# Performance work log

Hardware: AMD Instinct MI355X
Metric: run time of the kernel (lower is better)

The kernel has to match this reference:

```python
import jax, jax.numpy as jnp
import numpy as np

NUM_OUT_EDGES = 2
NUM_INTERMEDIATE = 2
NUM_FSM_STATES = NUM_OUT_EDGES + NUM_INTERMEDIATE  # S = 4
NUM_EDGE_TYPES = 3
NUM_VARIANTS = 4
NUM_NODE_TYPES = 8
NUM_NODES = 256
BACKTRACK_FAILS_PROB = 0.001
EDGE_PROB = 0.05  # avg degree ~ 12.8 per edge type


def setup_inputs() -> dict:
    key = jax.random.key(0)
    k1, k2, k3, k4 = jax.random.split(key, 4)
    vw = jax.random.uniform(k1, (NUM_NODES, NUM_NODES, NUM_VARIANTS))
    vw = vw / jnp.sum(vw, axis=-1, keepdims=True)  # nonneg, sums to 1 on last axis
    adjacency = (jax.random.uniform(k2, (NUM_EDGE_TYPES, NUM_NODES, NUM_NODES)) < EDGE_PROB).astype(jnp.float32)
    n_actions = NUM_EDGE_TYPES * NUM_FSM_STATES + 3  # moves + ACCEPT/BACKTRACK/FAIL
    log_routing_params = 0.5 * jax.random.normal(
        k3, (NUM_VARIANTS, NUM_NODE_TYPES, NUM_FSM_STATES, n_actions))
    node_types = jax.random.randint(k4, (NUM_NODES,), 0, NUM_NODE_TYPES)
    return {
        'variant_weights': vw,
        'adjacency': adjacency,
        'log_routing_params': log_routing_params,
        'node_types': node_types,
        'steps': 48,
    }


def _forward(variant_weights, adjacency, log_routing_params, node_types, steps):
    N = variant_weights.shape[0]
    S, T, E = NUM_FSM_STATES, NUM_EDGE_TYPES, NUM_OUT_EDGES
    dt = variant_weights.dtype

    # Row-normalized per-edge-type adjacency (uniform over typed successors;
    deg = jnp.sum(adjacency, axis=-1, keepdims=True)
    a_norm = adjacency / jnp.maximum(deg, 1.0)  # [T, N, N]

    # routing_softmax over actions; policy conditioned on (variant, node type, fsm state)
    policy = jax.nn.softmax(log_routing_params, axis=-1)  # [V, NT, S, A]
    pol_n = policy[:, node_types]                          # [V, N, S, A]

    # Mix policy variants per (start node i, current node j)
    mixed = jnp.einsum('ijv,vjsa->ijsa', variant_weights, pol_n)  # [N, N, S, A]
    p_move = mixed[..., :T * S].reshape(N, N, S, T, S)  # MOVE(edge type t, next state u)
    p_accept = mixed[..., T * S]                        # ACCEPT at current node
    p_back = mixed[..., T * S + 1]                      # BACKTRACK to start node

    # Start states: edge type e starts in fsm state e at node i (one-hot).
    eyeS = jnp.eye(S, dtype=dt)[:E]  # [E, S]
    eyeN = jnp.eye(N, dtype=dt)      # [N, N]
    dist0 = eyeS[:, None, :, None] * eyeN[None, :, None, :]  # [E, N, S, N]
    restart = dist0 * (1.0 - BACKTRACK_FAILS_PROB)

    def step(carry, _):
        dist, accept = carry  # dist: [E, N_start, S, N_cur], accept: [E, N, N]
        accept = accept + jnp.einsum('eisj,ijs->eij', dist, p_accept)
        back = jnp.einsum('eisj,ijs->ei', dist, p_back)
        tmp = jnp.einsum('eisj,ijstu->eituj', dist, p_move)   # pick edge type + next state
        moved = jnp.einsum('eituj,tjk->eiuk', tmp, a_norm)    # move along typed edges
        dist = moved + back[:, :, None, None] * restart
        return (dist, accept), None

    accept0 = jnp.zeros((E, N, N), dt)
    (dist, accept), _ = jax.lax.scan(step, (dist0, accept0), None, length=steps)
    # absorb remaining accept probability after final transition
    accept = accept + jnp.einsum('eisj,ijs->eij', dist, p_accept)
    return accept  # [num_out_edges, num_nodes, num_nodes]


def reference(variant_weights, adjacency, log_routing_params, node_types, steps):
    return _forward(variant_weights, adjacency, log_routing_params, node_types, steps)
```

## Files before the change

### kernel.cpp

```cpp
#include <hip/hip_runtime.h>
#include <hip/hip_fp16.h>

#define NN    256
#define SS    4
#define TT    3
#define VV    4
#define NTY   8
#define NAC   15
#define CAPG  48
#define CAPE  (CAPG * 2)
#define ROWB  40
#define ZROWB (NN * ROWB)
#define BUFB  (ZROWB + ROWB)
#define ZPK   ((unsigned)ZROWB | ((unsigned)ZROWB << 16))
#define GMR   16

typedef _Float16 h2v __attribute__((ext_vector_type(2)));

#if defined(__has_builtin)
#if __has_builtin(__builtin_amdgcn_fdot2)
#define HAVE_FDOT2 1
#endif
#endif

static __device__ __forceinline__ unsigned ph2(float a, float b) {
    union { __half2 h; unsigned u; } c;
    c.h = __floats2half2_rn(a, b);
    return c.u;
}
static __device__ __forceinline__ h2v bch2(unsigned u) {
    union { unsigned u; h2v h; } c; c.u = u; return c.h;
}
static __device__ __forceinline__ float2 h2f2(unsigned u) {
    union { unsigned u; __half2 h; } c; c.u = u; return __half22float2(c.h);
}

__global__ void k_setup(const float* __restrict__ adj,
                        const float* __restrict__ lrp,
                        float* __restrict__ inv_deg,
                        float* __restrict__ pol,
                        unsigned* __restrict__ epk,
                        int* __restrict__ gcnt) {
    const int b = blockIdx.x;
    const int tid = threadIdx.x;

    if (b < TT * NN) {
        __shared__ float wsum[4];
        float s = adj[(size_t)b * NN + tid];
#pragma unroll
        for (int off = 32; off > 0; off >>= 1) s += __shfl_down(s, off, 64);
        if ((tid & 63) == 0) wsum[tid >> 6] = s;
        __syncthreads();
        if (tid == 0)
            inv_deg[b] = 1.0f / fmaxf(wsum[0] + wsum[1] + wsum[2] + wsum[3], 1.0f);
    } else if (b < TT * NN + 64) {
        __shared__ int cnt[4];
        __shared__ unsigned short offs[4][CAPE + 2];
        const int c4 = (b - TT * NN) * 4;
        if (tid < 4) cnt[tid] = 0;
        __syncthreads();
#pragma unroll
        for (int t = 0; t < TT; t++) {
            const float4 a4 = *(const float4*)(adj + ((size_t)t * NN + tid) * NN + c4);
            const float av[4] = {a4.x, a4.y, a4.z, a4.w};
#pragma unroll
            for (int c = 0; c < 4; c++) {
                if (av[c] != 0.f) {
                    int idx = atomicAdd(&cnt[c], 1);
                    if (idx < CAPE) offs[c][idx] = (unsigned short)(tid * ROWB + t * 8);
                }
            }
        }
        __syncthreads();
        const int c    = tid >> 6;
        const int lane = tid & 63;
        int cc = cnt[c]; if (cc > CAPE) cc = CAPE;
        if (lane == 0 && (cc & 1)) offs[c][cc] = (unsigned short)ZROWB;
        __syncthreads();
        const int g = (cc + 1) >> 1;
        for (int gg = lane; gg < g; gg += 64)
            epk[(size_t)gg * NN + (c4 + c)] =
                (unsigned)offs[c][2 * gg] | ((unsigned)offs[c][2 * gg + 1] << 16);
        if (lane == 0) gcnt[c4 + c] = g;
    } else {
        if (tid < VV * NTY * SS) {
            float x[NAC]; float m = -3.4e38f;
#pragma unroll
            for (int a = 0; a < NAC; a++) { x[a] = lrp[tid * NAC + a]; m = fmaxf(m, x[a]); }
            float ssum = 0.f;
#pragma unroll
            for (int a = 0; a < NAC; a++) { x[a] = __expf(x[a] - m); ssum += x[a]; }
            float inv = 1.f / ssum;
#pragma unroll
            for (int a = 0; a < NAC; a++) pol[tid * NAC + a] = x[a] * inv;
        }
    }
}

__global__ __launch_bounds__(512, 4) void k_main(
    const float* __restrict__ vw,
    const int* __restrict__ node_types,
    const float* __restrict__ pol,
    const float* __restrict__ inv_deg,
    const unsigned* __restrict__ epk,
    const int* __restrict__ gcnt,
    const int* __restrict__ steps_p,
    float* __restrict__ out)
{
    const int i    = blockIdx.x & 255;
    const int e    = blockIdx.x >> 8;
    const int tid  = threadIdx.x;
    const int col  = tid >> 1;
    const int h    = tid & 1;
    const int lane = tid & 63;
    const int wv   = tid >> 6;
    const int steps = steps_p[0];

    __shared__ __align__(16) char tmpb[2 * BUFB];
    __shared__ __align__(16) float backp[2][8];

    if (tid < 20) {
        int pb = tid / 10, w = tid % 10;
        ((unsigned*)(tmpb + pb * BUFB + ZROWB))[w] = 0u;
    }

    const float4 w4 = *(const float4*)(vw + ((size_t)i * NN + col) * VV);
    const float wvv[VV] = {w4.x, w4.y, w4.z, w4.w};
    const int ntj = node_types[col];
    const int ab  = h * 6;
    float pm6[SS][6], pcb[SS];
#pragma unroll
    for (int s = 0; s < SS; s++) {
        pcb[s] = 0.f;
#pragma unroll
        for (int a = 0; a < 6; a++) pm6[s][a] = 0.f;
    }
#pragma unroll
    for (int v = 0; v < VV; v++) {
        const float* pr = pol + (size_t)(v * NTY + ntj) * SS * NAC;
#pragma unroll
        for (int s = 0; s < SS; s++) {
            const float* p = pr + s * NAC;
#pragma unroll
            for (int a = 0; a < 6; a++) pm6[s][a] = fmaf(wvv[v], p[ab + a], pm6[s][a]);
            pcb[s] = fmaf(wvv[v], p[12 + h], pcb[s]);
        }
    }
    {
        float invd[TT];
#pragma unroll
        for (int t = 0; t < TT; t++) invd[t] = inv_deg[t * NN + col];
#pragma unroll
        for (int s = 0; s < SS; s++)
#pragma unroll
            for (int a = 0; a < 6; a++) pm6[s][a] *= invd[(ab + a) >> 2];
    }

    float D0 = (0 == e && col == i) ? 1.f : 0.f;
    float D1 = (1 == e && col == i) ? 1.f : 0.f;
    float D2 = 0.f, D3 = 0.f;
    float acc = 0.f;

    const int g_all = gcnt[col];
    const int ch = (g_all - h + 1) >> 1;
    int km = ch;
#pragma unroll
    for (int off = 32; off > 0; off >>= 1) {
        int o = __shfl_xor(km, off, 64);
        km = o > km ? o : km;
    }
    const int kmax = __builtin_amdgcn_readfirstlane(km);

    unsigned ep[GMR];
#pragma unroll
    for (int k = 0; k < GMR; k++) {
        unsigned pk = epk[(size_t)(2 * k + h) * NN + col];
        ep[k] = (2 * k + h < g_all) ? pk : ZPK;
    }

    const h2v S10 = {(_Float16)1.0f, (_Float16)0.0f};
    const h2v S01 = {(_Float16)0.0f, (_Float16)1.0f};
    char* const myrow0 = tmpb + col * ROWB + h * 12;

    for (int step = 0; step < steps; step++) {
        const int par = step & 1;
        char* const buf = tmpb + par * BUFB;

        float r4 = D0 * pcb[0];
        r4 = fmaf(D1, pcb[1], r4); r4 = fmaf(D2, pcb[2], r4); r4 = fmaf(D3, pcb[3], r4);
        if (h == 0) acc += r4;
        float bj = h ? r4 : 0.f;

        float tv[6];
#pragma unroll
        for (int a = 0; a < 6; a++) {
            float x = D0 * pm6[0][a];
            x = fmaf(D1, pm6[1][a], x);
            x = fmaf(D2, pm6[2][a], x);
            x = fmaf(D3, pm6[3][a], x);
            tv[a] = x;
        }
        char* const myrow = myrow0 + par * BUFB;
        *(unsigned*)(myrow)     = ph2(tv[0], tv[1]);
        *(unsigned*)(myrow + 4) = ph2(tv[2], tv[3]);
        *(unsigned*)(myrow + 8) = ph2(tv[4], tv[5]);

#pragma unroll
        for (int off = 32; off > 0; off >>= 1) bj += __shfl_down(bj, off, 64);
        if (lane == 0) backp[par][wv] = bj;

        __syncthreads();

        float d0a = 0.f, d1a = 0.f, d2a = 0.f, d3a = 0.f;
        float d0b = 0.f, d1b = 0.f, d2b = 0.f, d3b = 0.f;
#pragma unroll
        for (int k = 0; k < GMR; k++) {
            if (k < kmax) {
                const unsigned pk = ep[k];
                const uint2 q0 = *(const uint2*)(buf + (pk & 0xffffu));
                const uint2 q1 = *(const uint2*)(buf + (pk >> 16));
#ifdef HAVE_FDOT2
                if (k & 1) {
                    d0b = __builtin_amdgcn_fdot2(bch2(q0.x), S10, d0b, false);
                    d1b = __builtin_amdgcn_fdot2(bch2(q0.x), S01, d1b, false);
                    d2b = __builtin_amdgcn_fdot2(bch2(q0.y), S10, d2b, false);
                    d3b = __builtin_amdgcn_fdot2(bch2(q0.y), S01, d3b, false);
                    d0b = __builtin_amdgcn_fdot2(bch2(q1.x), S10, d0b, false);
                    d1b = __builtin_amdgcn_fdot2(bch2(q1.x), S01, d1b, false);
                    d2b = __builtin_amdgcn_fdot2(bch2(q1.y), S10, d2b, false);
                    d3b = __builtin_amdgcn_fdot2(bch2(q1.y), S01, d3b, false);
                } else {
                    d0a = __builtin_amdgcn_fdot2(bch2(q0.x), S10, d0a, false);
                    d1a = __builtin_amdgcn_fdot2(bch2(q0.x), S01, d1a, false);
                    d2a = __builtin_amdgcn_fdot2(bch2(q0.y), S10, d2a, false);
                    d3a = __builtin_amdgcn_fdot2(bch2(q0.y), S01, d3a, false);
                    d0a = __builtin_amdgcn_fdot2(bch2(q1.x), S10, d0a, false);
                    d1a = __builtin_amdgcn_fdot2(bch2(q1.x), S01, d1a, false);
                    d2a = __builtin_amdgcn_fdot2(bch2(q1.y), S10, d2a, false);
                    d3a = __builtin_amdgcn_fdot2(bch2(q1.y), S01, d3a, false);
                }
#else
                float2 f0 = h2f2(q0.x), f1 = h2f2(q0.y), f2 = h2f2(q1.x), f3 = h2f2(q1.y);
                if (k & 1) {
                    d0b += f0.x + f2.x; d1b += f0.y + f2.y;
                    d2b += f1.x + f3.x; d3b += f1.y + f3.y;
                } else {
                    d0a += f0.x + f2.x; d1a += f0.y + f2.y;
                    d2a += f1.x + f3.x; d3a += f1.y + f3.y;
                }
#endif
            }
        }
        for (int k = GMR; k < kmax; k++) {
            unsigned pk = epk[(size_t)(2 * k + h) * NN + col];
            pk = (2 * k + h < g_all) ? pk : ZPK;
            const uint2 q0 = *(const uint2*)(buf + (pk & 0xffffu));
            const uint2 q1 = *(const uint2*)(buf + (pk >> 16));
            float2 f0 = h2f2(q0.x), f1 = h2f2(q0.y), f2 = h2f2(q1.x), f3 = h2f2(q1.y);
            d0a += f0.x + f2.x; d1a += f0.y + f2.y;
            d2a += f1.x + f3.x; d3a += f1.y + f3.y;
        }

        float d0 = d0a + d0b, d1 = d1a + d1b, d2 = d2a + d2b, d3 = d3a + d3b;

        d0 += __shfl_xor(d0, 1, 64);
        d1 += __shfl_xor(d1, 1, 64);
        d2 += __shfl_xor(d2, 1, 64);
        d3 += __shfl_xor(d3, 1, 64);

        const float4 b0 = *(const float4*)(&backp[par][0]);
        const float4 b1 = *(const float4*)(&backp[par][4]);
        const float back = ((b0.x + b0.y) + (b0.z + b0.w)) +
                           ((b1.x + b1.y) + (b1.z + b1.w));
        if (col == i) {
            if (e == 0) d0 = fmaf(back, 0.999f, d0);
            else        d1 = fmaf(back, 0.999f, d1);
        }
        D0 = d0; D1 = d1; D2 = d2; D3 = d3;
    }

    float r4 = D0 * pcb[0];
    r4 = fmaf(D1, pcb[1], r4); r4 = fmaf(D2, pcb[2], r4); r4 = fmaf(D3, pcb[3], r4);
    if (h == 0) {
        acc += r4;
        out[((size_t)e * NN + i) * NN + col] = acc;
    }
}

extern "C" void kernel_launch(void* const* d_in, const int* in_sizes, int n_in,
                              void* d_out, int out_size, void* d_ws, size_t ws_size,
                              hipStream_t stream) {
    const float* vw  = (const float*)d_in[0];
    const float* adj = (const float*)d_in[1];
    const float* lrp = (const float*)d_in[2];
    const int* node_types = (const int*)d_in[3];
    const int* steps_p    = (const int*)d_in[4];

    float* ws       = (float*)d_ws;
    float* pol      = ws;
    float* inv_deg  = ws + 1920;
    int*   gcnt     = (int*)(ws + 2688);
    unsigned* epk   = (unsigned*)(ws + 2944);

    k_setup<<<TT * NN + 64 + 1, 256, 0, stream>>>(adj, lrp, inv_deg, pol, epk, gcnt);
    k_main<<<2 * NN, 512, 0, stream>>>(vw, node_types, pol, inv_deg, epk, gcnt,
                                       steps_p, (float*)d_out);
}
```

Measured before the change: 166.6 us.

## Split each destination column across four threads instead of two

Moves from 2 to 4 threads per column (1024-thread blocks). Three lanes each handle one edge type's move probabilities and edge-group gathers, and the fourth computes the accept and backtrack terms. This shortens each thread's serial per-step gather chain and spreads the work over more waves. The cost is an extra cross-lane shuffle round, a larger block-wide barrier and fewer registers per thread.

```diff
diff --git a/kernel.cpp b/kernel.cpp
--- a/kernel.cpp
+++ b/kernel.cpp
@@ -13,7 +13,7 @@
 #define ZROWB (NN * ROWB)
 #define BUFB  (ZROWB + ROWB)
 #define ZPK   ((unsigned)ZROWB | ((unsigned)ZROWB << 16))
-#define GMR   16
+#define GMR4  8
 
 typedef _Float16 h2v __attribute__((ext_vector_type(2)));
 
@@ -97,7 +97,7 @@
     }
 }
 
-__global__ __launch_bounds__(512, 4) void k_main(
+__global__ __launch_bounds__(1024, 8) void k_main(
     const float* __restrict__ vw,
     const int* __restrict__ node_types,
     const float* __restrict__ pol,
@@ -110,14 +110,14 @@
     const int i    = blockIdx.x & 255;
     const int e    = blockIdx.x >> 8;
     const int tid  = threadIdx.x;
-    const int col  = tid >> 1;
-    const int h    = tid & 1;
+    const int col  = tid >> 2;
+    const int h    = tid & 3;
     const int lane = tid & 63;
     const int wv   = tid >> 6;
     const int steps = steps_p[0];
 
     __shared__ __align__(16) char tmpb[2 * BUFB];
-    __shared__ __align__(16) float backp[2][8];
+    __shared__ __align__(16) float backp[2][16];
 
     if (tid < 20) {
         int pb = tid / 10, w = tid % 10;
@@ -127,14 +127,14 @@
     const float4 w4 = *(const float4*)(vw + ((size_t)i * NN + col) * VV);
     const float wvv[VV] = {w4.x, w4.y, w4.z, w4.w};
     const int ntj = node_types[col];
-    const int ab  = h * 6;
-    float pm6[SS][6], pcb[SS];
-#pragma unroll
-    for (int s = 0; s < SS; s++) {
-        pcb[s] = 0.f;
-#pragma unroll
-        for (int a = 0; a < 6; a++) pm6[s][a] = 0.f;
-    }
+    int ai[4];
+    if (h < 3) { ai[0] = 4 * h; ai[1] = 4 * h + 1; ai[2] = 4 * h + 2; ai[3] = 4 * h + 3; }
+    else       { ai[0] = 12;    ai[1] = 13;        ai[2] = 14;        ai[3] = 14;        }
+    float pm[SS][4];
+#pragma unroll
+    for (int s = 0; s < SS; s++)
+#pragma unroll
+        for (int u = 0; u < 4; u++) pm[s][u] = 0.f;
 #pragma unroll
     for (int v = 0; v < VV; v++) {
         const float* pr = pol + (size_t)(v * NTY + ntj) * SS * NAC;
@@ -142,18 +142,16 @@
         for (int s = 0; s < SS; s++) {
             const float* p = pr + s * NAC;
 #pragma unroll
-            for (int a = 0; a < 6; a++) pm6[s][a] = fmaf(wvv[v], p[ab + a], pm6[s][a]);
-            pcb[s] = fmaf(wvv[v], p[12 + h], pcb[s]);
+            for (int u = 0; u < 4; u++) pm[s][u] = fmaf(wvv[v], p[ai[u]], pm[s][u]);
         }
     }
     {
-        float invd[TT];
-#pragma unroll
-        for (int t = 0; t < TT; t++) invd[t] = inv_deg[t * NN + col];
+        float invd = 1.f;
+        if (h < 3) invd = inv_deg[h * NN + col];
 #pragma unroll
         for (int s = 0; s < SS; s++)
 #pragma unroll
-            for (int a = 0; a < 6; a++) pm6[s][a] *= invd[(ab + a) >> 2];
+            for (int u = 0; u < 4; u++) pm[s][u] *= invd;
     }
 
     float D0 = (0 == e && col == i) ? 1.f : 0.f;
@@ -162,7 +160,7 @@
     float acc = 0.f;
 
     const int g_all = gcnt[col];
-    const int ch = (g_all - h + 1) >> 1;
+    const int ch = (g_all - h + 3) >> 2;
     int km = ch;
 #pragma unroll
     for (int off = 32; off > 0; off >>= 1) {
@@ -171,39 +169,36 @@
     }
     const int kmax = __builtin_amdgcn_readfirstlane(km);
 
-    unsigned ep[GMR];
-#pragma unroll
-    for (int k = 0; k < GMR; k++) {
-        unsigned pk = epk[(size_t)(2 * k + h) * NN + col];
-        ep[k] = (2 * k + h < g_all) ? pk : ZPK;
+    unsigned ep[GMR4];
+#pragma unroll
+    for (int k = 0; k < GMR4; k++) {
+        unsigned pk = epk[(size_t)(4 * k + h) * NN + col];
+        ep[k] = (4 * k + h < g_all) ? pk : ZPK;
     }
 
     const h2v S10 = {(_Float16)1.0f, (_Float16)0.0f};
     const h2v S01 = {(_Float16)0.0f, (_Float16)1.0f};
-    char* const myrow0 = tmpb + col * ROWB + h * 12;
+    char* const myrow0 = tmpb + col * ROWB + h * 8;
 
     for (int step = 0; step < steps; step++) {
         const int par = step & 1;
         char* const buf = tmpb + par * BUFB;
 
-        float r4 = D0 * pcb[0];
-        r4 = fmaf(D1, pcb[1], r4); r4 = fmaf(D2, pcb[2], r4); r4 = fmaf(D3, pcb[3], r4);
-        if (h == 0) acc += r4;
-        float bj = h ? r4 : 0.f;
-
-        float tv[6];
-#pragma unroll
-        for (int a = 0; a < 6; a++) {
-            float x = D0 * pm6[0][a];
-            x = fmaf(D1, pm6[1][a], x);
-            x = fmaf(D2, pm6[2][a], x);
-            x = fmaf(D3, pm6[3][a], x);
-            tv[a] = x;
-        }
-        char* const myrow = myrow0 + par * BUFB;
-        *(unsigned*)(myrow)     = ph2(tv[0], tv[1]);
-        *(unsigned*)(myrow + 4) = ph2(tv[2], tv[3]);
-        *(unsigned*)(myrow + 8) = ph2(tv[4], tv[5]);
+        float tv0 = D0 * pm[0][0];
+        tv0 = fmaf(D1, pm[1][0], tv0); tv0 = fmaf(D2, pm[2][0], tv0); tv0 = fmaf(D3, pm[3][0], tv0);
+        float tv1 = D0 * pm[0][1];
+        tv1 = fmaf(D1, pm[1][1], tv1); tv1 = fmaf(D2, pm[2][1], tv1); tv1 = fmaf(D3, pm[3][1], tv1);
+        float tv2 = D0 * pm[0][2];
+        tv2 = fmaf(D1, pm[1][2], tv2); tv2 = fmaf(D2, pm[2][2], tv2); tv2 = fmaf(D3, pm[3][2], tv2);
+        float tv3 = D0 * pm[0][3];
+        tv3 = fmaf(D1, pm[1][3], tv3); tv3 = fmaf(D2, pm[2][3], tv3); tv3 = fmaf(D3, pm[3][3], tv3);
+
+        float bj = 0.f;
+        if (h == 3) { acc += tv0; bj = tv1; }
+        else {
+            uint2 w; w.x = ph2(tv0, tv1); w.y = ph2(tv2, tv3);
+            *(uint2*)(myrow0 + par * BUFB) = w;
+        }
 
 #pragma unroll
         for (int off = 32; off > 0; off >>= 1) bj += __shfl_down(bj, off, 64);
@@ -214,7 +209,7 @@
         float d0a = 0.f, d1a = 0.f, d2a = 0.f, d3a = 0.f;
         float d0b = 0.f, d1b = 0.f, d2b = 0.f, d3b = 0.f;
 #pragma unroll
-        for (int k = 0; k < GMR; k++) {
+        for (int k = 0; k < GMR4; k++) {
             if (k < kmax) {
                 const unsigned pk = ep[k];
                 const uint2 q0 = *(const uint2*)(buf + (pk & 0xffffu));
@@ -251,9 +246,9 @@
 #endif
             }
         }
-        for (int k = GMR; k < kmax; k++) {
-            unsigned pk = epk[(size_t)(2 * k + h) * NN + col];
-            pk = (2 * k + h < g_all) ? pk : ZPK;
+        for (int k = GMR4; k < kmax; k++) {
+            unsigned pk = epk[(size_t)(4 * k + h) * NN + col];
+            pk = (4 * k + h < g_all) ? pk : ZPK;
             const uint2 q0 = *(const uint2*)(buf + (pk & 0xffffu));
             const uint2 q1 = *(const uint2*)(buf + (pk >> 16));
             float2 f0 = h2f2(q0.x), f1 = h2f2(q0.y), f2 = h2f2(q1.x), f3 = h2f2(q1.y);
@@ -263,15 +258,19 @@
 
         float d0 = d0a + d0b, d1 = d1a + d1b, d2 = d2a + d2b, d3 = d3a + d3b;
 
-        d0 += __shfl_xor(d0, 1, 64);
-        d1 += __shfl_xor(d1, 1, 64);
-        d2 += __shfl_xor(d2, 1, 64);
-        d3 += __shfl_xor(d3, 1, 64);
+        d0 += __shfl_xor(d0, 1, 64);  d0 += __shfl_xor(d0, 2, 64);
+        d1 += __shfl_xor(d1, 1, 64);  d1 += __shfl_xor(d1, 2, 64);
+        d2 += __shfl_xor(d2, 1, 64);  d2 += __shfl_xor(d2, 2, 64);
+        d3 += __shfl_xor(d3, 1, 64);  d3 += __shfl_xor(d3, 2, 64);
 
         const float4 b0 = *(const float4*)(&backp[par][0]);
         const float4 b1 = *(const float4*)(&backp[par][4]);
-        const float back = ((b0.x + b0.y) + (b0.z + b0.w)) +
-                           ((b1.x + b1.y) + (b1.z + b1.w));
+        const float4 b2 = *(const float4*)(&backp[par][8]);
+        const float4 b3 = *(const float4*)(&backp[par][12]);
+        const float back = (((b0.x + b0.y) + (b0.z + b0.w)) +
+                            ((b1.x + b1.y) + (b1.z + b1.w))) +
+                           (((b2.x + b2.y) + (b2.z + b2.w)) +
+                            ((b3.x + b3.y) + (b3.z + b3.w)));
         if (col == i) {
             if (e == 0) d0 = fmaf(back, 0.999f, d0);
             else        d1 = fmaf(back, 0.999f, d1);
@@ -279,10 +278,10 @@
         D0 = d0; D1 = d1; D2 = d2; D3 = d3;
     }
 
-    float r4 = D0 * pcb[0];
-    r4 = fmaf(D1, pcb[1], r4); r4 = fmaf(D2, pcb[2], r4); r4 = fmaf(D3, pcb[3], r4);
-    if (h == 0) {
-        acc += r4;
+    if (h == 3) {
+        float r = D0 * pm[0][0];
+        r = fmaf(D1, pm[1][0], r); r = fmaf(D2, pm[2][0], r); r = fmaf(D3, pm[3][0], r);
+        acc += r;
         out[((size_t)e * NN + i) * NN + col] = acc;
     }
 }
@@ -303,6 +302,6 @@
     unsigned* epk   = (unsigned*)(ws + 2944);
 
     k_setup<<<TT * NN + 64 + 1, 256, 0, stream>>>(adj, lrp, inv_deg, pol, epk, gcnt);
-    k_main<<<2 * NN, 512, 0, stream>>>(vw, node_types, pol, inv_deg, epk, gcnt,
-                                       steps_p, (float*)d_out);
-}
+    k_main<<<2 * NN, 1024, 0, stream>>>(vw, node_types, pol, inv_deg, epk, gcnt,
+                                        steps_p, (float*)d_out);
+}
```

Result: slower. 222.4 us (+33.5%).

## Sort columns by edge-group count to cut wavefront divergence in gather loop

Applied to the files above, without the earlier changes.

Adds a small counting-sort kernel that orders the destination columns by their gathered-edge group count and uses that permutation to assign columns to threads. Threads in a wavefront then run similar loop trip counts, which cuts divergence in the sparse gather-accumulate loop. The unrolled gather loop now handles two edge groups per iteration with separate accumulators to expose more LDS loads in flight, and the back-probability read is moved inside the diagonal branch. The cost is an extra kernel launch, an indirection load per thread, and scattered output stores; pairing iterations also assumes that reading ep[kc+1] is safe when kmax is odd.

```diff
diff --git a/kernel.cpp b/kernel.cpp
--- a/kernel.cpp
+++ b/kernel.cpp
@@ -97,6 +97,24 @@
     }
 }
 
+__global__ void k_sort(const int* __restrict__ gcnt, int* __restrict__ perm) {
+    __shared__ int base[64];
+    const int tid = threadIdx.x;
+    if (tid < 64) base[tid] = 0;
+    __syncthreads();
+    const int g = gcnt[tid] & 63;
+    atomicAdd(&base[g], 1);
+    __syncthreads();
+    if (tid == 0) {
+        int s = 0;
+#pragma unroll
+        for (int b = 0; b < 64; b++) { int c = base[b]; base[b] = s; s += c; }
+    }
+    __syncthreads();
+    const int pos = atomicAdd(&base[g], 1);
+    perm[pos] = tid;
+}
+
 __global__ __launch_bounds__(512, 4) void k_main(
     const float* __restrict__ vw,
     const int* __restrict__ node_types,
@@ -104,13 +122,14 @@
     const float* __restrict__ inv_deg,
     const unsigned* __restrict__ epk,
     const int* __restrict__ gcnt,
+    const int* __restrict__ perm,
     const int* __restrict__ steps_p,
     float* __restrict__ out)
 {
     const int i    = blockIdx.x & 255;
     const int e    = blockIdx.x >> 8;
     const int tid  = threadIdx.x;
-    const int col  = tid >> 1;
+    const int col  = perm[tid >> 1];
     const int h    = tid & 1;
     const int lane = tid & 63;
     const int wv   = tid >> 6;
@@ -214,40 +233,38 @@
         float d0a = 0.f, d1a = 0.f, d2a = 0.f, d3a = 0.f;
         float d0b = 0.f, d1b = 0.f, d2b = 0.f, d3b = 0.f;
 #pragma unroll
-        for (int k = 0; k < GMR; k++) {
-            if (k < kmax) {
-                const unsigned pk = ep[k];
-                const uint2 q0 = *(const uint2*)(buf + (pk & 0xffffu));
-                const uint2 q1 = *(const uint2*)(buf + (pk >> 16));
+        for (int kc = 0; kc < GMR; kc += 2) {
+            if (kc < kmax) {
+                const unsigned pkA = ep[kc];
+                const unsigned pkB = ep[kc + 1];
+                const uint2 qA0 = *(const uint2*)(buf + (pkA & 0xffffu));
+                const uint2 qA1 = *(const uint2*)(buf + (pkA >> 16));
+                const uint2 qB0 = *(const uint2*)(buf + (pkB & 0xffffu));
+                const uint2 qB1 = *(const uint2*)(buf + (pkB >> 16));
 #ifdef HAVE_FDOT2
-                if (k & 1) {
-                    d0b = __builtin_amdgcn_fdot2(bch2(q0.x), S10, d0b, false);
-                    d1b = __builtin_amdgcn_fdot2(bch2(q0.x), S01, d1b, false);
-                    d2b = __builtin_amdgcn_fdot2(bch2(q0.y), S10, d2b, false);
-                    d3b = __builtin_amdgcn_fdot2(bch2(q0.y), S01, d3b, false);
-                    d0b = __builtin_amdgcn_fdot2(bch2(q1.x), S10, d0b, false);
-                    d1b = __builtin_amdgcn_fdot2(bch2(q1.x), S01, d1b, false);
-                    d2b = __builtin_amdgcn_fdot2(bch2(q1.y), S10, d2b, false);
-                    d3b = __builtin_amdgcn_fdot2(bch2(q1.y), S01, d3b, false);
-                } else {
-                    d0a = __builtin_amdgcn_fdot2(bch2(q0.x), S10, d0a, false);
-                    d1a = __builtin_amdgcn_fdot2(bch2(q0.x), S01, d1a, false);
-                    d2a = __builtin_amdgcn_fdot2(bch2(q0.y), S10, d2a, false);
-                    d3a = __builtin_amdgcn_fdot2(bch2(q0.y), S01, d3a, false);
-                    d0a = __builtin_amdgcn_fdot2(bch2(q1.x), S10, d0a, false);
-                    d1a = __builtin_amdgcn_fdot2(bch2(q1.x), S01, d1a, false);
-                    d2a = __builtin_amdgcn_fdot2(bch2(q1.y), S10, d2a, false);
-                    d3a = __builtin_amdgcn_fdot2(bch2(q1.y), S01, d3a, false);
-                }
+                d0a = __builtin_amdgcn_fdot2(bch2(qA0.x), S10, d0a, false);
+                d1a = __builtin_amdgcn_fdot2(bch2(qA0.x), S01, d1a, false);
+                d2a = __builtin_amdgcn_fdot2(bch2(qA0.y), S10, d2a, false);
+                d3a = __builtin_amdgcn_fdot2(bch2(qA0.y), S01, d3a, false);
+                d0a = __builtin_amdgcn_fdot2(bch2(qA1.x), S10, d0a, false);
+                d1a = __builtin_amdgcn_fdot2(bch2(qA1.x), S01, d1a, false);
+                d2a = __builtin_amdgcn_fdot2(bch2(qA1.y), S10, d2a, false);
+                d3a = __builtin_amdgcn_fdot2(bch2(qA1.y), S01, d3a, false);
+                d0b = __builtin_amdgcn_fdot2(bch2(qB0.x), S10, d0b, false);
+                d1b = __builtin_amdgcn_fdot2(bch2(qB0.x), S01, d1b, false);
+                d2b = __builtin_amdgcn_fdot2(bch2(qB0.y), S10, d2b, false);
+                d3b = __builtin_amdgcn_fdot2(bch2(qB0.y), S01, d3b, false);
+                d0b = __builtin_amdgcn_fdot2(bch2(qB1.x), S10, d0b, false);
+                d1b = __builtin_amdgcn_fdot2(bch2(qB1.x), S01, d1b, false);
+                d2b = __builtin_amdgcn_fdot2(bch2(qB1.y), S10, d2b, false);
+                d3b = __builtin_amdgcn_fdot2(bch2(qB1.y), S01, d3b, false);
 #else
-                float2 f0 = h2f2(q0.x), f1 = h2f2(q0.y), f2 = h2f2(q1.x), f3 = h2f2(q1.y);
-                if (k & 1) {
-                    d0b += f0.x + f2.x; d1b += f0.y + f2.y;
-                    d2b += f1.x + f3.x; d3b += f1.y + f3.y;
-                } else {
-                    d0a += f0.x + f2.x; d1a += f0.y + f2.y;
-                    d2a += f1.x + f3.x; d3a += f1.y + f3.y;
-                }
+                float2 f0 = h2f2(qA0.x), f1 = h2f2(qA0.y), f2 = h2f2(qA1.x), f3 = h2f2(qA1.y);
+                d0a += f0.x + f2.x; d1a += f0.y + f2.y;
+                d2a += f1.x + f3.x; d3a += f1.y + f3.y;
+                float2 g0 = h2f2(qB0.x), g1 = h2f2(qB0.y), g2 = h2f2(qB1.x), g3 = h2f2(qB1.y);
+                d0b += g0.x + g2.x; d1b += g0.y + g2.y;
+                d2b += g1.x + g3.x; d3b += g1.y + g3.y;
 #endif
             }
         }
@@ -268,11 +285,11 @@
         d2 += __shfl_xor(d2, 1, 64);
         d3 += __shfl_xor(d3, 1, 64);
 
-        const float4 b0 = *(const float4*)(&backp[par][0]);
-        const float4 b1 = *(const float4*)(&backp[par][4]);
-        const float back = ((b0.x + b0.y) + (b0.z + b0.w)) +
-                           ((b1.x + b1.y) + (b1.z + b1.w));
         if (col == i) {
+            const float4 b0 = *(const float4*)(&backp[par][0]);
+            const float4 b1 = *(const float4*)(&backp[par][4]);
+            const float back = ((b0.x + b0.y) + (b0.z + b0.w)) +
+                               ((b1.x + b1.y) + (b1.z + b1.w));
             if (e == 0) d0 = fmaf(back, 0.999f, d0);
             else        d1 = fmaf(back, 0.999f, d1);
         }
@@ -301,8 +318,10 @@
     float* inv_deg  = ws + 1920;
     int*   gcnt     = (int*)(ws + 2688);
     unsigned* epk   = (unsigned*)(ws + 2944);
+    int*   perm     = (int*)(ws + 2944 + CAPG * NN);
 
     k_setup<<<TT * NN + 64 + 1, 256, 0, stream>>>(adj, lrp, inv_deg, pol, epk, gcnt);
+    k_sort<<<1, 256, 0, stream>>>(gcnt, perm);
     k_main<<<2 * NN, 512, 0, stream>>>(vw, node_types, pol, inv_deg, epk, gcnt,
-                                       steps_p, (float*)d_out);
-}
+                                       perm, steps_p, (float*)d_out);
+}
```

Result: no change. 163.4 us (-1.9%).
